# Performance work log

Measured on AMD Instinct MI355X. Metric: run time of the kernel, lower is better.

The kernel has to match this reference:

```python
import jax, jax.numpy as jnp
import numpy as np

E = 8      # num_experts
D = 1024   # input_size
H = 1024   # head_size
K = 2      # top-k


def setup_inputs() -> dict:
    key = jax.random.key(0)
    k1, k2, k3, k4, k5, k6 = jax.random.split(key, 6)
    x = jax.random.normal(k1, (4, 1024, D), dtype=jnp.float32)
    # ParallelExperts init: uniform(-1/fan_in, 1/fan_in)
    w1 = jax.random.uniform(k2, (E, D, H), jnp.float32, -1.0 / D, 1.0 / D)
    b1 = jax.random.uniform(k3, (E, H), jnp.float32, -1.0 / np.sqrt(D), 1.0 / np.sqrt(D))
    w2 = jax.random.uniform(k4, (E, H, D), jnp.float32, -1.0 / H, 1.0 / H)
    b2 = jax.random.uniform(k5, (E, D), jnp.float32, -1.0 / np.sqrt(H), 1.0 / np.sqrt(H))
    # gate Linear(input_size, num_experts, bias=False); scaled so softmax isn't saturated
    wg = jax.random.normal(k6, (D, E), dtype=jnp.float32) * 0.02
    return {"x": x, "w1": w1, "b1": b1, "w2": w2, "b2": b2, "wg": wg}


def reference(x, w1, b1, w2, b2, wg):
    bsz, length, d = x.shape
    xf = x.reshape(-1, d)                                  # [T, D]
    # --- top_k_gating (noisy_gating=False, no skip_mask) ---
    logits = xf @ wg                                       # [T, E]
    probs = jax.nn.softmax(logits, axis=-1)
    top_v, top_i = jax.lax.top_k(probs, K)                 # [T, K]
    top_v = top_v / (jnp.sum(top_v, axis=-1, keepdims=True) + 1e-6)
    # dense combine weights: gate[t, e] = renormalized prob if e in top-k else 0
    gates = jnp.sum(jax.nn.one_hot(top_i, E, dtype=xf.dtype) * top_v[..., None], axis=1)  # [T, E]
    # --- map: per-expert first GEMM + bias (dense formulation == grouped GEMM, no drops) ---
    h = jnp.einsum('td,edh->teh', xf, w1) + b1[None]       # [T, E, H]
    # --- activation between map and reduce (nn.GELU, exact erf form) ---
    a = jax.nn.gelu(h, approximate=False)
    # --- reduce: per-expert second GEMM + bias, scaled by gate, scatter-add back ---
    o = jnp.einsum('teh,ehd->ted', a, w2) + b2[None]       # [T, E, D]
    y = jnp.einsum('te,ted->td', gates, o)                 # [T, D]
    return y.reshape(bsz, length, d)
```

## Files before the change

### kernel.cpp

```cpp
#include <hip/hip_runtime.h>
#include <hip/hip_bf16.h>
#include <math.h>

#define TT 4096
#define EE 8
#define DD 1024
#define HH 1024
#define CAP 4096

typedef __attribute__((ext_vector_type(8))) short bf16x8;
typedef __attribute__((ext_vector_type(4))) float f32x4;

#define GLL16(gp, lp)                                                                   \
    __builtin_amdgcn_global_load_lds((__attribute__((address_space(1))) void*)(gp),     \
                                     (__attribute__((address_space(3))) void*)(lp),     \
                                     16, 0, 0)

static const size_t OFF_XB     = 0;
static const size_t OFF_W1T    = 8u * 1024 * 1024;
static const size_t OFF_W2T    = 24u * 1024 * 1024;
static const size_t OFF_ABUF   = 40u * 1024 * 1024;
static const size_t OFF_OBUF   = 56u * 1024 * 1024;
static const size_t OFF_ROWMAP = 88u * 1024 * 1024;
static const size_t OFF_GATES  = OFF_ROWMAP + 8 * CAP * 4;
static const size_t OFF_COUNTS = OFF_GATES + 8192 * 4;
static const size_t OFF_PICKS  = OFF_COUNTS + 256;

__global__ __launch_bounds__(256) void prep_kernel(
    const float* __restrict__ x, const float* __restrict__ wg,
    const float* __restrict__ w1, const float* __restrict__ w2,
    __hip_bfloat16* __restrict__ xb,
    __hip_bfloat16* __restrict__ w1t, __hip_bfloat16* __restrict__ w2t,
    int* __restrict__ picks, float* __restrict__ gates)
{
    __shared__ float tl[64][65];
    const int bid = blockIdx.x;
    const int tid = threadIdx.x;

    if (bid < 4096) {
        const int mat = bid >> 8;
        const int tt = bid & 255;
        const int R = (tt >> 4) * 64;
        const int C = (tt & 15) * 64;
        const float* src = (mat < EE ? w1 : w2) + (size_t)(mat & 7) * DD * HH;
        __hip_bfloat16* dst = (mat < EE ? w1t : w2t) + (size_t)(mat & 7) * DD * HH;

        const int lrow = tid >> 4;
        const int c4 = tid & 15;
#pragma unroll
        for (int i = 0; i < 4; ++i) {
            const int r = lrow + i * 16;
            float4 v = *(const float4*)(src + (size_t)(R + r) * 1024 + C + c4 * 4);
            tl[r][c4 * 4 + 0] = v.x;
            tl[r][c4 * 4 + 1] = v.y;
            tl[r][c4 * 4 + 2] = v.z;
            tl[r][c4 * 4 + 3] = v.w;
        }
        __syncthreads();
        const int seg = tid & 7;
        const int orow0 = tid >> 3;
#pragma unroll
        for (int p = 0; p < 2; ++p) {
            const int orow = orow0 + p * 32;
            unsigned short u[8];
#pragma unroll
            for (int j = 0; j < 8; ++j) {
                __hip_bfloat16 h = __float2bfloat16(tl[seg * 8 + j][orow]);
                u[j] = *(unsigned short*)&h;
            }
            *(ushort4*)(dst + (size_t)(C + orow) * 1024 + R + seg * 8)     = (ushort4){u[0], u[1], u[2], u[3]};
            *(ushort4*)(dst + (size_t)(C + orow) * 1024 + R + seg * 8 + 4) = (ushort4){u[4], u[5], u[6], u[7]};
        }
        return;
    }

    const int lane = tid & 63;
    const int wave = tid >> 6;
    const int tbase = (bid - 4096) * 16 + wave * 4;

    for (int i = 0; i < 4; ++i) {
        const int t = tbase + i;
        const float4* xr = (const float4*)(x + (size_t)t * DD);
        ushort4* xbr = (ushort4*)(xb + (size_t)t * DD);

        float acc[EE];
#pragma unroll
        for (int e = 0; e < EE; ++e) acc[e] = 0.f;

#pragma unroll
        for (int c = 0; c < 4; ++c) {
            const int v4 = lane + 64 * c;
            float4 xv = xr[v4];
            __hip_bfloat16 h0 = __float2bfloat16(xv.x);
            __hip_bfloat16 h1 = __float2bfloat16(xv.y);
            __hip_bfloat16 h2 = __float2bfloat16(xv.z);
            __hip_bfloat16 h3 = __float2bfloat16(xv.w);
            ushort4 s;
            s.x = *(unsigned short*)&h0; s.y = *(unsigned short*)&h1;
            s.z = *(unsigned short*)&h2; s.w = *(unsigned short*)&h3;
            xbr[v4] = s;
            const float4* wrow = (const float4*)(wg + (size_t)(4 * v4) * EE);
            const float xs[4] = {xv.x, xv.y, xv.z, xv.w};
#pragma unroll
            for (int q = 0; q < 4; ++q) {
                float4 w0 = wrow[q * 2];
                float4 w1v = wrow[q * 2 + 1];
                acc[0] = fmaf(xs[q], w0.x, acc[0]);
                acc[1] = fmaf(xs[q], w0.y, acc[1]);
                acc[2] = fmaf(xs[q], w0.z, acc[2]);
                acc[3] = fmaf(xs[q], w0.w, acc[3]);
                acc[4] = fmaf(xs[q], w1v.x, acc[4]);
                acc[5] = fmaf(xs[q], w1v.y, acc[5]);
                acc[6] = fmaf(xs[q], w1v.z, acc[6]);
                acc[7] = fmaf(xs[q], w1v.w, acc[7]);
            }
        }
#pragma unroll
        for (int off = 32; off > 0; off >>= 1) {
#pragma unroll
            for (int e = 0; e < EE; ++e) acc[e] += __shfl_xor(acc[e], off, 64);
        }
        if (lane == 0) {
            float mx = acc[0];
#pragma unroll
            for (int e = 1; e < EE; ++e) mx = fmaxf(mx, acc[e]);
            float p[EE];
            float s = 0.f;
#pragma unroll
            for (int e = 0; e < EE; ++e) { p[e] = expf(acc[e] - mx); s += p[e]; }
            int i0 = 0;
#pragma unroll
            for (int e = 1; e < EE; ++e) if (acc[e] > acc[i0]) i0 = e;
            int i1 = (i0 == 0) ? 1 : 0;
#pragma unroll
            for (int e = 0; e < EE; ++e) {
                if (e != i0 && acc[e] > acc[i1]) i1 = e;
            }
            float v0 = p[i0] / s, v1 = p[i1] / s;
            float den = v0 + v1 + 1e-6f;
            gates[t * 2 + 0] = v0 / den;
            gates[t * 2 + 1] = v1 / den;
            picks[t] = i0 | (i1 << 4);
        }
    }
}

__global__ __launch_bounds__(256) void bucket_build(
    const int* __restrict__ picks, int* __restrict__ rowmap, int* __restrict__ counts)
{
    const int e = blockIdx.x;
    const int tid = threadIdx.x;
    const int lane = tid & 63;
    const int wave = tid >> 6;
    __shared__ int wsum[4];

    int runtot = 0;
    for (int tb = 0; tb < TT; tb += 256) {
        const int t = tb + tid;
        const int p = picks[t];
        const int m0 = ((p & 15) == e) ? 1 : 0;
        const int m1 = (((p >> 4) & 15) == e) ? 1 : 0;
        const int c = m0 + m1;
        int incl = c;
#pragma unroll
        for (int off = 1; off < 64; off <<= 1) {
            int v = __shfl_up(incl, off, 64);
            if (lane >= off) incl += v;
        }
        if (lane == 63) wsum[wave] = incl;
        __syncthreads();
        int wbase = 0;
#pragma unroll
        for (int w = 0; w < 4; ++w) wbase += (w < wave) ? wsum[w] : 0;
        int slot = runtot + wbase + incl - c;
        if (m0) { rowmap[e * CAP + slot] = t * 2; slot += 1; }
        if (m1) { rowmap[e * CAP + slot] = t * 2 + 1; }
        runtot += wsum[0] + wsum[1] + wsum[2] + wsum[3];
        __syncthreads();
    }
    if (tid == 0) counts[e] = runtot;
}

template <int LAYER>
__global__ __launch_bounds__(256) void moe_gemm(
    const __hip_bfloat16* __restrict__ Abase,
    const __hip_bfloat16* __restrict__ Bbase,
    const float* __restrict__ bias,
    const int* __restrict__ rowmap,
    const int* __restrict__ counts,
    const float* __restrict__ gates,
    void* __restrict__ OutP)
{
    const int e = blockIdx.z;
    const int cnt = counts[e];
    const int m0 = blockIdx.y * 128;
    if (m0 >= cnt) return;
    const int n0 = blockIdx.x * 128;
    const int tid = threadIdx.x;
    const int lane = tid & 63;
    const int wave = tid >> 6;
    const int wm = (wave >> 1) * 64;
    const int wn = (wave & 1) * 64;
    const int lrow = lane & 15;
    const int quad = lane >> 4;

    __shared__ __hip_bfloat16 As[4][128 * 32];
    __shared__ __hip_bfloat16 Bs[4][128 * 32];

    const int ar0 = m0 + (tid >> 2);
    const int ar1 = ar0 + 64;
    const int e0 = rowmap[e * CAP + (ar0 < cnt ? ar0 : 0)];
    const int e1 = rowmap[e * CAP + (ar1 < cnt ? ar1 : 0)];
    const size_t src0 = (size_t)(LAYER == 1 ? (e0 >> 1) : e0);
    const size_t src1 = (size_t)(LAYER == 1 ? (e1 >> 1) : e1);
    const __hip_bfloat16* gA0 = Abase + src0 * DD + (tid & 3) * 8;
    const __hip_bfloat16* gA1 = Abase + src1 * DD + (tid & 3) * 8;
    const __hip_bfloat16* Bexp = Bbase + (size_t)e * DD * HH;
    const __hip_bfloat16* gB0 = Bexp + (size_t)(n0 + (tid >> 2)) * DD + (tid & 3) * 8;
    const __hip_bfloat16* gB1 = gB0 + (size_t)64 * DD;

    f32x4 acc[4][4];
#pragma unroll
    for (int i = 0; i < 4; ++i)
#pragma unroll
        for (int j = 0; j < 4; ++j) acc[i][j] = (f32x4){0.f, 0.f, 0.f, 0.f};

    for (int kt = 0; kt < DD / 128; ++kt) {
#pragma unroll
        for (int s = 0; s < 4; ++s) {
            const int ko = kt * 128 + s * 32;
            char* lA = (char*)&As[s][0] + wave * 1024;
            char* lB = (char*)&Bs[s][0] + wave * 1024;
            GLL16(gA0 + ko, lA);
            GLL16(gA1 + ko, lA + 4096);
            GLL16(gB0 + ko, lB);
            GLL16(gB1 + ko, lB + 4096);
        }
        __syncthreads();

#pragma unroll
        for (int s = 0; s < 4; ++s) {
            const bf16x8* Av = (const bf16x8*)&As[s][0];
            const bf16x8* Bv = (const bf16x8*)&Bs[s][0];
            bf16x8 af[4], bfr[4];
#pragma unroll
            for (int i = 0; i < 4; ++i) {
                af[i]  = Av[(wm + i * 16 + lrow) * 4 + quad];
                bfr[i] = Bv[(wn + i * 16 + lrow) * 4 + quad];
            }
#pragma unroll
            for (int mi = 0; mi < 4; ++mi)
#pragma unroll
                for (int ni = 0; ni < 4; ++ni)
                    acc[mi][ni] = __builtin_amdgcn_mfma_f32_16x16x32_bf16(
                        af[mi], bfr[ni], acc[mi][ni], 0, 0, 0);
        }
        __syncthreads();
    }

    if (LAYER == 1) {
        __hip_bfloat16* abuf = (__hip_bfloat16*)OutP;
#pragma unroll
        for (int mi = 0; mi < 4; ++mi) {
#pragma unroll
            for (int r = 0; r < 4; ++r) {
                const int mrow = wm + mi * 16 + quad * 4 + r;
                const int gm = m0 + mrow;
                if (gm < cnt) {
                    const int ent = rowmap[e * CAP + gm];
                    __hip_bfloat16* orow = abuf + (size_t)ent * HH + n0 + wn + lrow;
#pragma unroll
                    for (int ni = 0; ni < 4; ++ni) {
                        float v = acc[mi][ni][r] + bias[e * HH + n0 + wn + ni * 16 + lrow];
                        v = 0.5f * v * (1.f + erff(v * 0.70710678118654752f));
                        orow[ni * 16] = __float2bfloat16(v);
                    }
                }
            }
        }
    } else {
        float* obuf = (float*)OutP;
#pragma unroll
        for (int mi = 0; mi < 4; ++mi) {
#pragma unroll
            for (int r = 0; r < 4; ++r) {
                const int mrow = wm + mi * 16 + quad * 4 + r;
                const int gm = m0 + mrow;
                if (gm < cnt) {
                    const int ent = rowmap[e * CAP + gm];
                    const float g = gates[ent];
                    float* orow = obuf + (size_t)ent * DD + n0 + wn + lrow;
#pragma unroll
                    for (int ni = 0; ni < 4; ++ni) {
                        float v = acc[mi][ni][r] + bias[e * DD + n0 + wn + ni * 16 + lrow];
                        orow[ni * 16] = v * g;
                    }
                }
            }
        }
    }
}

__global__ __launch_bounds__(256) void combine_kernel(
    const float* __restrict__ obuf, float* __restrict__ y)
{
    const size_t i = (size_t)blockIdx.x * 256 + threadIdx.x;
    const size_t t = i >> 8;
    const size_t c = i & 255;
    const float4* o0 = (const float4*)(obuf + t * 2 * DD);
    float4 a = o0[c];
    float4 b = o0[256 + c];
    float4 r;
    r.x = a.x + b.x; r.y = a.y + b.y; r.z = a.z + b.z; r.w = a.w + b.w;
    ((float4*)y)[i] = r;
}

extern "C" void kernel_launch(void* const* d_in, const int* in_sizes, int n_in,
                              void* d_out, int out_size, void* d_ws, size_t ws_size,
                              hipStream_t stream)
{
    const float* x  = (const float*)d_in[0];
    const float* w1 = (const float*)d_in[1];
    const float* b1 = (const float*)d_in[2];
    const float* w2 = (const float*)d_in[3];
    const float* b2 = (const float*)d_in[4];
    const float* wg = (const float*)d_in[5];
    float* y = (float*)d_out;

    char* ws = (char*)d_ws;
    __hip_bfloat16* xb   = (__hip_bfloat16*)(ws + OFF_XB);
    __hip_bfloat16* w1t  = (__hip_bfloat16*)(ws + OFF_W1T);
    __hip_bfloat16* w2t  = (__hip_bfloat16*)(ws + OFF_W2T);
    __hip_bfloat16* abuf = (__hip_bfloat16*)(ws + OFF_ABUF);
    float* obuf  = (float*)(ws + OFF_OBUF);
    int*   rowmap = (int*)(ws + OFF_ROWMAP);
    float* gates  = (float*)(ws + OFF_GATES);
    int*   counts = (int*)(ws + OFF_COUNTS);
    int*   picks  = (int*)(ws + OFF_PICKS);

    prep_kernel<<<4096 + 256, 256, 0, stream>>>(x, wg, w1, w2, xb, w1t, w2t, picks, gates);
    bucket_build<<<EE, 256, 0, stream>>>(picks, rowmap, counts);
    moe_gemm<1><<<dim3(HH / 128, CAP / 128, EE), 256, 0, stream>>>(
        xb, w1t, b1, rowmap, counts, gates, (void*)abuf);
    moe_gemm<2><<<dim3(DD / 128, CAP / 128, EE), 256, 0, stream>>>(
        abuf, w2t, b2, rowmap, counts, gates, (void*)obuf);
    combine_kernel<<<TT * DD / 4 / 256, 256, 0, stream>>>(obuf, y);
}
```

Measured before the change: 257.0 us.

## Use single-wave register-direct GEMM tiles and atomically combine experts into output

Replaces the 256-thread, 128x128 LDS-staged GEMM with a 64-thread, 64x64 tile in which each wave loads its MFMA fragments straight from global memory into registers, double-buffered across k-steps, with no shared memory or barriers. The second GEMM now atomically adds gated expert outputs into y, which is zeroed up front, so the intermediate obuf and the combine kernel are dropped. This removes barrier stalls and a full write and read of the intermediate buffer. In exchange, operands are no longer reused through LDS and global loads become less coalesced, the grid has four times as many blocks, and float atomics add contention and make the summation order nondeterministic.

```diff
diff --git a/kernel.cpp b/kernel.cpp
--- a/kernel.cpp
+++ b/kernel.cpp
@@ -11,16 +11,10 @@
 typedef __attribute__((ext_vector_type(8))) short bf16x8;
 typedef __attribute__((ext_vector_type(4))) float f32x4;
 
-#define GLL16(gp, lp)                                                                   \
-    __builtin_amdgcn_global_load_lds((__attribute__((address_space(1))) void*)(gp),     \
-                                     (__attribute__((address_space(3))) void*)(lp),     \
-                                     16, 0, 0)
-
 static const size_t OFF_XB     = 0;
 static const size_t OFF_W1T    = 8u * 1024 * 1024;
 static const size_t OFF_W2T    = 24u * 1024 * 1024;
 static const size_t OFF_ABUF   = 40u * 1024 * 1024;
-static const size_t OFF_OBUF   = 56u * 1024 * 1024;
 static const size_t OFF_ROWMAP = 88u * 1024 * 1024;
 static const size_t OFF_GATES  = OFF_ROWMAP + 8 * CAP * 4;
 static const size_t OFF_COUNTS = OFF_GATES + 8192 * 4;
@@ -182,7 +176,7 @@
 }
 
 template <int LAYER>
-__global__ __launch_bounds__(256) void moe_gemm(
+__global__ __launch_bounds__(64) void moe_gemm(
     const __hip_bfloat16* __restrict__ Abase,
     const __hip_bfloat16* __restrict__ Bbase,
     const float* __restrict__ bias,
@@ -193,31 +187,24 @@
 {
     const int e = blockIdx.z;
     const int cnt = counts[e];
-    const int m0 = blockIdx.y * 128;
+    const int m0 = blockIdx.y * 64;
     if (m0 >= cnt) return;
-    const int n0 = blockIdx.x * 128;
-    const int tid = threadIdx.x;
-    const int lane = tid & 63;
-    const int wave = tid >> 6;
-    const int wm = (wave >> 1) * 64;
-    const int wn = (wave & 1) * 64;
+    const int n0 = blockIdx.x * 64;
+    const int lane = threadIdx.x;
     const int lrow = lane & 15;
     const int quad = lane >> 4;
 
-    __shared__ __hip_bfloat16 As[4][128 * 32];
-    __shared__ __hip_bfloat16 Bs[4][128 * 32];
-
-    const int ar0 = m0 + (tid >> 2);
-    const int ar1 = ar0 + 64;
-    const int e0 = rowmap[e * CAP + (ar0 < cnt ? ar0 : 0)];
-    const int e1 = rowmap[e * CAP + (ar1 < cnt ? ar1 : 0)];
-    const size_t src0 = (size_t)(LAYER == 1 ? (e0 >> 1) : e0);
-    const size_t src1 = (size_t)(LAYER == 1 ? (e1 >> 1) : e1);
-    const __hip_bfloat16* gA0 = Abase + src0 * DD + (tid & 3) * 8;
-    const __hip_bfloat16* gA1 = Abase + src1 * DD + (tid & 3) * 8;
     const __hip_bfloat16* Bexp = Bbase + (size_t)e * DD * HH;
-    const __hip_bfloat16* gB0 = Bexp + (size_t)(n0 + (tid >> 2)) * DD + (tid & 3) * 8;
-    const __hip_bfloat16* gB1 = gB0 + (size_t)64 * DD;
+    const __hip_bfloat16* ap[4];
+    const __hip_bfloat16* bp[4];
+#pragma unroll
+    for (int i = 0; i < 4; ++i) {
+        const int gm = m0 + i * 16 + lrow;
+        const int ent = rowmap[e * CAP + (gm < cnt ? gm : 0)];
+        const size_t src = (size_t)(LAYER == 1 ? (ent >> 1) : ent);
+        ap[i] = Abase + src * DD + quad * 8;
+        bp[i] = Bexp + (size_t)(n0 + i * 16 + lrow) * DD + quad * 8;
+    }
 
     f32x4 acc[4][4];
 #pragma unroll
@@ -225,38 +212,32 @@
 #pragma unroll
         for (int j = 0; j < 4; ++j) acc[i][j] = (f32x4){0.f, 0.f, 0.f, 0.f};
 
-    for (int kt = 0; kt < DD / 128; ++kt) {
-#pragma unroll
-        for (int s = 0; s < 4; ++s) {
-            const int ko = kt * 128 + s * 32;
-            char* lA = (char*)&As[s][0] + wave * 1024;
-            char* lB = (char*)&Bs[s][0] + wave * 1024;
-            GLL16(gA0 + ko, lA);
-            GLL16(gA1 + ko, lA + 4096);
-            GLL16(gB0 + ko, lB);
-            GLL16(gB1 + ko, lB + 4096);
-        }
-        __syncthreads();
-
-#pragma unroll
-        for (int s = 0; s < 4; ++s) {
-            const bf16x8* Av = (const bf16x8*)&As[s][0];
-            const bf16x8* Bv = (const bf16x8*)&Bs[s][0];
-            bf16x8 af[4], bfr[4];
-#pragma unroll
-            for (int i = 0; i < 4; ++i) {
-                af[i]  = Av[(wm + i * 16 + lrow) * 4 + quad];
-                bfr[i] = Bv[(wn + i * 16 + lrow) * 4 + quad];
-            }
-#pragma unroll
-            for (int mi = 0; mi < 4; ++mi)
-#pragma unroll
-                for (int ni = 0; ni < 4; ++ni)
-                    acc[mi][ni] = __builtin_amdgcn_mfma_f32_16x16x32_bf16(
-                        af[mi], bfr[ni], acc[mi][ni], 0, 0, 0);
-        }
-        __syncthreads();
-    }
+    bf16x8 aF[2][4], bF[2][4];
+#define LOADF(S, KO)                                                       \
+    {                                                                      \
+        _Pragma("unroll") for (int i = 0; i < 4; ++i) {                    \
+            aF[S][i] = *(const bf16x8*)(ap[i] + (KO));                     \
+            bF[S][i] = *(const bf16x8*)(bp[i] + (KO));                     \
+        }                                                                  \
+    }
+#define MM(S)                                                              \
+    {                                                                      \
+        _Pragma("unroll") for (int mi = 0; mi < 4; ++mi)                   \
+            _Pragma("unroll") for (int ni = 0; ni < 4; ++ni)               \
+                acc[mi][ni] = __builtin_amdgcn_mfma_f32_16x16x32_bf16(     \
+                    aF[S][mi], bF[S][ni], acc[mi][ni], 0, 0, 0);           \
+    }
+
+    LOADF(0, 0);
+#pragma unroll 4
+    for (int it = 0; it < 16; ++it) {
+        LOADF(1, 64 * it + 32);
+        MM(0);
+        LOADF(0, 64 * it + 64);
+        MM(1);
+    }
+#undef LOADF
+#undef MM
 
     if (LAYER == 1) {
         __hip_bfloat16* abuf = (__hip_bfloat16*)OutP;
@@ -264,14 +245,13 @@
         for (int mi = 0; mi < 4; ++mi) {
 #pragma unroll
             for (int r = 0; r < 4; ++r) {
-                const int mrow = wm + mi * 16 + quad * 4 + r;
-                const int gm = m0 + mrow;
+                const int gm = m0 + mi * 16 + quad * 4 + r;
                 if (gm < cnt) {
                     const int ent = rowmap[e * CAP + gm];
-                    __hip_bfloat16* orow = abuf + (size_t)ent * HH + n0 + wn + lrow;
+                    __hip_bfloat16* orow = abuf + (size_t)ent * HH + n0 + lrow;
 #pragma unroll
                     for (int ni = 0; ni < 4; ++ni) {
-                        float v = acc[mi][ni][r] + bias[e * HH + n0 + wn + ni * 16 + lrow];
+                        float v = acc[mi][ni][r] + bias[e * HH + n0 + ni * 16 + lrow];
                         v = 0.5f * v * (1.f + erff(v * 0.70710678118654752f));
                         orow[ni * 16] = __float2bfloat16(v);
                     }
@@ -279,40 +259,26 @@
             }
         }
     } else {
-        float* obuf = (float*)OutP;
+        float* y = (float*)OutP;
 #pragma unroll
         for (int mi = 0; mi < 4; ++mi) {
 #pragma unroll
             for (int r = 0; r < 4; ++r) {
-                const int mrow = wm + mi * 16 + quad * 4 + r;
-                const int gm = m0 + mrow;
+                const int gm = m0 + mi * 16 + quad * 4 + r;
                 if (gm < cnt) {
                     const int ent = rowmap[e * CAP + gm];
                     const float g = gates[ent];
-                    float* orow = obuf + (size_t)ent * DD + n0 + wn + lrow;
+                    const int t = ent >> 1;
+                    float* yrow = y + (size_t)t * DD + n0 + lrow;
 #pragma unroll
                     for (int ni = 0; ni < 4; ++ni) {
-                        float v = acc[mi][ni][r] + bias[e * DD + n0 + wn + ni * 16 + lrow];
-                        orow[ni * 16] = v * g;
+                        float v = acc[mi][ni][r] + bias[e * DD + n0 + ni * 16 + lrow];
+                        atomicAdd(yrow + ni * 16, v * g);
                     }
                 }
             }
         }
     }
-}
-
-__global__ __launch_bounds__(256) void combine_kernel(
-    const float* __restrict__ obuf, float* __restrict__ y)
-{
-    const size_t i = (size_t)blockIdx.x * 256 + threadIdx.x;
-    const size_t t = i >> 8;
-    const size_t c = i & 255;
-    const float4* o0 = (const float4*)(obuf + t * 2 * DD);
-    float4 a = o0[c];
-    float4 b = o0[256 + c];
-    float4 r;
-    r.x = a.x + b.x; r.y = a.y + b.y; r.z = a.z + b.z; r.w = a.w + b.w;
-    ((float4*)y)[i] = r;
 }
 
 extern "C" void kernel_launch(void* const* d_in, const int* in_sizes, int n_in,
@@ -332,17 +298,16 @@
     __hip_bfloat16* w1t  = (__hip_bfloat16*)(ws + OFF_W1T);
     __hip_bfloat16* w2t  = (__hip_bfloat16*)(ws + OFF_W2T);
     __hip_bfloat16* abuf = (__hip_bfloat16*)(ws + OFF_ABUF);
-    float* obuf  = (float*)(ws + OFF_OBUF);
     int*   rowmap = (int*)(ws + OFF_ROWMAP);
     float* gates  = (float*)(ws + OFF_GATES);
     int*   counts = (int*)(ws + OFF_COUNTS);
     int*   picks  = (int*)(ws + OFF_PICKS);
 
+    hipMemsetAsync(y, 0, (size_t)TT * DD * sizeof(float), stream);
     prep_kernel<<<4096 + 256, 256, 0, stream>>>(x, wg, w1, w2, xb, w1t, w2t, picks, gates);
     bucket_build<<<EE, 256, 0, stream>>>(picks, rowmap, counts);
-    moe_gemm<1><<<dim3(HH / 128, CAP / 128, EE), 256, 0, stream>>>(
+    moe_gemm<1><<<dim3(HH / 64, CAP / 64, EE), 64, 0, stream>>>(
         xb, w1t, b1, rowmap, counts, gates, (void*)abuf);
-    moe_gemm<2><<<dim3(DD / 128, CAP / 128, EE), 256, 0, stream>>>(
-        abuf, w2t, b2, rowmap, counts, gates, (void*)obuf);
-    combine_kernel<<<TT * DD / 4 / 256, 256, 0, stream>>>(obuf, y);
+    moe_gemm<2><<<dim3(DD / 64, CAP / 64, EE), 64, 0, stream>>>(
+        abuf, w2t, b2, rowmap, counts, gates, (void*)y);
 }
```

After: 370.8 us. +44.3%, slower.

## Double-buffer GEMM k-loop and fuse top-k combine via atomic adds

Applied to the files above, without the earlier changes.

The GEMM main loop moves from loading four 32-wide k-slices then computing, with two barriers per 128-k step, to a double-buffered pipeline. Each iteration issues the next 32-wide slice while computing the current one, using half the LDS. The second GEMM also atomically adds gate-scaled outputs straight into y, which is zeroed with a memset, so the intermediate fp32 buffer and the combine kernel go away. This trades one barrier per 32-k slice and float atomics, whose summation order is nondeterministic, for less memory traffic and one fewer launch.

```diff
diff --git a/kernel.cpp b/kernel.cpp
--- a/kernel.cpp
+++ b/kernel.cpp
@@ -20,7 +20,6 @@
 static const size_t OFF_W1T    = 8u * 1024 * 1024;
 static const size_t OFF_W2T    = 24u * 1024 * 1024;
 static const size_t OFF_ABUF   = 40u * 1024 * 1024;
-static const size_t OFF_OBUF   = 56u * 1024 * 1024;
 static const size_t OFF_ROWMAP = 88u * 1024 * 1024;
 static const size_t OFF_GATES  = OFF_ROWMAP + 8 * CAP * 4;
 static const size_t OFF_COUNTS = OFF_GATES + 8192 * 4;
@@ -204,8 +203,8 @@
     const int lrow = lane & 15;
     const int quad = lane >> 4;
 
-    __shared__ __hip_bfloat16 As[4][128 * 32];
-    __shared__ __hip_bfloat16 Bs[4][128 * 32];
+    __shared__ __hip_bfloat16 As[2][128 * 32];
+    __shared__ __hip_bfloat16 Bs[2][128 * 32];
 
     const int ar0 = m0 + (tid >> 2);
     const int ar1 = ar0 + 64;
@@ -225,38 +224,40 @@
 #pragma unroll
         for (int j = 0; j < 4; ++j) acc[i][j] = (f32x4){0.f, 0.f, 0.f, 0.f};
 
-    for (int kt = 0; kt < DD / 128; ++kt) {
-#pragma unroll
-        for (int s = 0; s < 4; ++s) {
-            const int ko = kt * 128 + s * 32;
-            char* lA = (char*)&As[s][0] + wave * 1024;
-            char* lB = (char*)&Bs[s][0] + wave * 1024;
-            GLL16(gA0 + ko, lA);
-            GLL16(gA1 + ko, lA + 4096);
-            GLL16(gB0 + ko, lB);
-            GLL16(gB1 + ko, lB + 4096);
-        }
+#define STAGE(BUF, KO)                                              \
+    {                                                               \
+        char* lA = (char*)&As[BUF][0] + wave * 1024;                \
+        char* lB = (char*)&Bs[BUF][0] + wave * 1024;                \
+        GLL16(gA0 + (KO), lA);                                      \
+        GLL16(gA1 + (KO), lA + 4096);                               \
+        GLL16(gB0 + (KO), lB);                                      \
+        GLL16(gB1 + (KO), lB + 4096);                               \
+    }
+
+    STAGE(0, 0);
+    __syncthreads();
+
+    for (int kt = 0; kt < DD / 32; ++kt) {
+        const int cur = kt & 1;
+        if (kt < DD / 32 - 1) STAGE(cur ^ 1, (kt + 1) * 32);
+
+        const bf16x8* Av = (const bf16x8*)&As[cur][0];
+        const bf16x8* Bv = (const bf16x8*)&Bs[cur][0];
+        bf16x8 af[4], bfr[4];
+#pragma unroll
+        for (int i = 0; i < 4; ++i) {
+            af[i]  = Av[(wm + i * 16 + lrow) * 4 + quad];
+            bfr[i] = Bv[(wn + i * 16 + lrow) * 4 + quad];
+        }
+#pragma unroll
+        for (int mi = 0; mi < 4; ++mi)
+#pragma unroll
+            for (int ni = 0; ni < 4; ++ni)
+                acc[mi][ni] = __builtin_amdgcn_mfma_f32_16x16x32_bf16(
+                    af[mi], bfr[ni], acc[mi][ni], 0, 0, 0);
         __syncthreads();
-
-#pragma unroll
-        for (int s = 0; s < 4; ++s) {
-            const bf16x8* Av = (const bf16x8*)&As[s][0];
-            const bf16x8* Bv = (const bf16x8*)&Bs[s][0];
-            bf16x8 af[4], bfr[4];
-#pragma unroll
-            for (int i = 0; i < 4; ++i) {
-                af[i]  = Av[(wm + i * 16 + lrow) * 4 + quad];
-                bfr[i] = Bv[(wn + i * 16 + lrow) * 4 + quad];
-            }
-#pragma unroll
-            for (int mi = 0; mi < 4; ++mi)
-#pragma unroll
-                for (int ni = 0; ni < 4; ++ni)
-                    acc[mi][ni] = __builtin_amdgcn_mfma_f32_16x16x32_bf16(
-                        af[mi], bfr[ni], acc[mi][ni], 0, 0, 0);
-        }
-        __syncthreads();
-    }
+    }
+#undef STAGE
 
     if (LAYER == 1) {
         __hip_bfloat16* abuf = (__hip_bfloat16*)OutP;
@@ -279,7 +280,7 @@
             }
         }
     } else {
-        float* obuf = (float*)OutP;
+        float* y = (float*)OutP;
 #pragma unroll
         for (int mi = 0; mi < 4; ++mi) {
 #pragma unroll
@@ -289,30 +290,17 @@
                 if (gm < cnt) {
                     const int ent = rowmap[e * CAP + gm];
                     const float g = gates[ent];
-                    float* orow = obuf + (size_t)ent * DD + n0 + wn + lrow;
+                    const int t = ent >> 1;
+                    float* yrow = y + (size_t)t * DD + n0 + wn + lrow;
 #pragma unroll
                     for (int ni = 0; ni < 4; ++ni) {
                         float v = acc[mi][ni][r] + bias[e * DD + n0 + wn + ni * 16 + lrow];
-                        orow[ni * 16] = v * g;
+                        atomicAdd(yrow + ni * 16, v * g);
                     }
                 }
             }
         }
     }
-}
-
-__global__ __launch_bounds__(256) void combine_kernel(
-    const float* __restrict__ obuf, float* __restrict__ y)
-{
-    const size_t i = (size_t)blockIdx.x * 256 + threadIdx.x;
-    const size_t t = i >> 8;
-    const size_t c = i & 255;
-    const float4* o0 = (const float4*)(obuf + t * 2 * DD);
-    float4 a = o0[c];
-    float4 b = o0[256 + c];
-    float4 r;
-    r.x = a.x + b.x; r.y = a.y + b.y; r.z = a.z + b.z; r.w = a.w + b.w;
-    ((float4*)y)[i] = r;
 }
 
 extern "C" void kernel_launch(void* const* d_in, const int* in_sizes, int n_in,
@@ -332,17 +320,16 @@
     __hip_bfloat16* w1t  = (__hip_bfloat16*)(ws + OFF_W1T);
     __hip_bfloat16* w2t  = (__hip_bfloat16*)(ws + OFF_W2T);
     __hip_bfloat16* abuf = (__hip_bfloat16*)(ws + OFF_ABUF);
-    float* obuf  = (float*)(ws + OFF_OBUF);
     int*   rowmap = (int*)(ws + OFF_ROWMAP);
     float* gates  = (float*)(ws + OFF_GATES);
     int*   counts = (int*)(ws + OFF_COUNTS);
     int*   picks  = (int*)(ws + OFF_PICKS);
 
+    hipMemsetAsync(y, 0, (size_t)TT * DD * sizeof(float), stream);
     prep_kernel<<<4096 + 256, 256, 0, stream>>>(x, wg, w1, w2, xb, w1t, w2t, picks, gates);
     bucket_build<<<EE, 256, 0, stream>>>(picks, rowmap, counts);
     moe_gemm<1><<<dim3(HH / 128, CAP / 128, EE), 256, 0, stream>>>(
         xb, w1t, b1, rowmap, counts, gates, (void*)abuf);
     moe_gemm<2><<<dim3(DD / 128, CAP / 128, EE), 256, 0, stream>>>(
-        abuf, w2t, b2, rowmap, counts, gates, (void*)obuf);
-    combine_kernel<<<TT * DD / 4 / 256, 256, 0, stream>>>(obuf, y);
+        abuf, w2t, b2, rowmap, counts, gates, (void*)y);
 }
```

Measured after the change: 274.6 us. +6.8%, slower.

## Shrink MoE GEMM N-tile to 64 and use 64-wide K stages

Applied to the files above, without the earlier changes.

The grouped GEMM tile goes from 128x128 to 128x64, with each wave computing 64x32. The K loop now loads a single 64-wide K slab per barrier pair instead of four 32-wide slabs. The LDS load mapping is rewritten so each wave gathers 32 A rows and 16 B rows with 8 lanes per row. The smaller tile and LDS footprint give twice as many blocks and better occupancy for the ~8192 routed rows, at the cost of lower arithmetic intensity per block and twice as many barrier iterations.

```diff
diff --git a/kernel.cpp b/kernel.cpp
--- a/kernel.cpp
+++ b/kernel.cpp
@@ -195,63 +195,66 @@
     const int cnt = counts[e];
     const int m0 = blockIdx.y * 128;
     if (m0 >= cnt) return;
-    const int n0 = blockIdx.x * 128;
+    const int n0 = blockIdx.x * 64;
     const int tid = threadIdx.x;
     const int lane = tid & 63;
     const int wave = tid >> 6;
     const int wm = (wave >> 1) * 64;
-    const int wn = (wave & 1) * 64;
+    const int wn = (wave & 1) * 32;
     const int lrow = lane & 15;
     const int quad = lane >> 4;
 
-    __shared__ __hip_bfloat16 As[4][128 * 32];
-    __shared__ __hip_bfloat16 Bs[4][128 * 32];
-
-    const int ar0 = m0 + (tid >> 2);
-    const int ar1 = ar0 + 64;
-    const int e0 = rowmap[e * CAP + (ar0 < cnt ? ar0 : 0)];
-    const int e1 = rowmap[e * CAP + (ar1 < cnt ? ar1 : 0)];
-    const size_t src0 = (size_t)(LAYER == 1 ? (e0 >> 1) : e0);
-    const size_t src1 = (size_t)(LAYER == 1 ? (e1 >> 1) : e1);
-    const __hip_bfloat16* gA0 = Abase + src0 * DD + (tid & 3) * 8;
-    const __hip_bfloat16* gA1 = Abase + src1 * DD + (tid & 3) * 8;
+    __shared__ __hip_bfloat16 As[128 * 64];
+    __shared__ __hip_bfloat16 Bs[64 * 64];
+
     const __hip_bfloat16* Bexp = Bbase + (size_t)e * DD * HH;
-    const __hip_bfloat16* gB0 = Bexp + (size_t)(n0 + (tid >> 2)) * DD + (tid & 3) * 8;
-    const __hip_bfloat16* gB1 = gB0 + (size_t)64 * DD;
-
-    f32x4 acc[4][4];
+    const __hip_bfloat16* gA[4];
+    const __hip_bfloat16* gB[2];
+#pragma unroll
+    for (int j = 0; j < 4; ++j) {
+        const int gm = m0 + 32 * wave + 8 * j + (lane >> 3);
+        const int ent = rowmap[e * CAP + (gm < cnt ? gm : 0)];
+        const size_t src = (size_t)(LAYER == 1 ? (ent >> 1) : ent);
+        gA[j] = Abase + src * DD + (lane & 7) * 8;
+    }
+#pragma unroll
+    for (int j = 0; j < 2; ++j) {
+        const int gn = n0 + 16 * wave + 8 * j + (lane >> 3);
+        gB[j] = Bexp + (size_t)gn * DD + (lane & 7) * 8;
+    }
+    char* ldsA = (char*)As + wave * 4096;
+    char* ldsB = (char*)Bs + wave * 2048;
+
+    f32x4 acc[4][2];
 #pragma unroll
     for (int i = 0; i < 4; ++i)
 #pragma unroll
-        for (int j = 0; j < 4; ++j) acc[i][j] = (f32x4){0.f, 0.f, 0.f, 0.f};
-
-    for (int kt = 0; kt < DD / 128; ++kt) {
-#pragma unroll
-        for (int s = 0; s < 4; ++s) {
-            const int ko = kt * 128 + s * 32;
-            char* lA = (char*)&As[s][0] + wave * 1024;
-            char* lB = (char*)&Bs[s][0] + wave * 1024;
-            GLL16(gA0 + ko, lA);
-            GLL16(gA1 + ko, lA + 4096);
-            GLL16(gB0 + ko, lB);
-            GLL16(gB1 + ko, lB + 4096);
-        }
-        __syncthreads();
-
-#pragma unroll
-        for (int s = 0; s < 4; ++s) {
-            const bf16x8* Av = (const bf16x8*)&As[s][0];
-            const bf16x8* Bv = (const bf16x8*)&Bs[s][0];
-            bf16x8 af[4], bfr[4];
-#pragma unroll
-            for (int i = 0; i < 4; ++i) {
-                af[i]  = Av[(wm + i * 16 + lrow) * 4 + quad];
-                bfr[i] = Bv[(wn + i * 16 + lrow) * 4 + quad];
-            }
+        for (int j = 0; j < 2; ++j) acc[i][j] = (f32x4){0.f, 0.f, 0.f, 0.f};
+
+    const bf16x8* Av = (const bf16x8*)As;
+    const bf16x8* Bv = (const bf16x8*)Bs;
+
+    for (int kt = 0; kt < DD / 64; ++kt) {
+        const int ko = kt * 64;
+#pragma unroll
+        for (int j = 0; j < 4; ++j) GLL16(gA[j] + ko, ldsA + j * 1024);
+#pragma unroll
+        for (int j = 0; j < 2; ++j) GLL16(gB[j] + ko, ldsB + j * 1024);
+        __syncthreads();
+
+#pragma unroll
+        for (int s = 0; s < 2; ++s) {
+            bf16x8 af[4], bfr[2];
+#pragma unroll
+            for (int i = 0; i < 4; ++i)
+                af[i] = Av[(wm + i * 16 + lrow) * 8 + quad + 4 * s];
+#pragma unroll
+            for (int i = 0; i < 2; ++i)
+                bfr[i] = Bv[(wn + i * 16 + lrow) * 8 + quad + 4 * s];
 #pragma unroll
             for (int mi = 0; mi < 4; ++mi)
 #pragma unroll
-                for (int ni = 0; ni < 4; ++ni)
+                for (int ni = 0; ni < 2; ++ni)
                     acc[mi][ni] = __builtin_amdgcn_mfma_f32_16x16x32_bf16(
                         af[mi], bfr[ni], acc[mi][ni], 0, 0, 0);
         }
@@ -270,7 +273,7 @@
                     const int ent = rowmap[e * CAP + gm];
                     __hip_bfloat16* orow = abuf + (size_t)ent * HH + n0 + wn + lrow;
 #pragma unroll
-                    for (int ni = 0; ni < 4; ++ni) {
+                    for (int ni = 0; ni < 2; ++ni) {
                         float v = acc[mi][ni][r] + bias[e * HH + n0 + wn + ni * 16 + lrow];
                         v = 0.5f * v * (1.f + erff(v * 0.70710678118654752f));
                         orow[ni * 16] = __float2bfloat16(v);
@@ -291,7 +294,7 @@
                     const float g = gates[ent];
                     float* orow = obuf + (size_t)ent * DD + n0 + wn + lrow;
 #pragma unroll
-                    for (int ni = 0; ni < 4; ++ni) {
+                    for (int ni = 0; ni < 2; ++ni) {
                         float v = acc[mi][ni][r] + bias[e * DD + n0 + wn + ni * 16 + lrow];
                         orow[ni * 16] = v * g;
                     }
@@ -340,9 +343,9 @@
 
     prep_kernel<<<4096 + 256, 256, 0, stream>>>(x, wg, w1, w2, xb, w1t, w2t, picks, gates);
     bucket_build<<<EE, 256, 0, stream>>>(picks, rowmap, counts);
-    moe_gemm<1><<<dim3(HH / 128, CAP / 128, EE), 256, 0, stream>>>(
+    moe_gemm<1><<<dim3(HH / 64, CAP / 128, EE), 256, 0, stream>>>(
         xb, w1t, b1, rowmap, counts, gates, (void*)abuf);
-    moe_gemm<2><<<dim3(DD / 128, CAP / 128, EE), 256, 0, stream>>>(
+    moe_gemm<2><<<dim3(DD / 64, CAP / 128, EE), 256, 0, stream>>>(
         abuf, w2t, b2, rowmap, counts, gates, (void*)obuf);
     combine_kernel<<<TT * DD / 4 / 256, 256, 0, stream>>>(obuf, y);
 }
```

Result: faster. 243.3 us (-5.3%).
